# Optimization experiments

Hardware: AMD Instinct MI355X
Metric: run time of the kernel (lower is better)

The kernel has to match this reference:

```python
import jax, jax.numpy as jnp
import numpy as np
import math

B, N, C, S, H, E = 2, 20000, 512, 128, 8, 320000
D = C // H
EPS = 1e-6


def setup_inputs() -> dict:
    key = jax.random.key(0)
    ks = jax.random.split(key, 14)
    x = jax.random.normal(ks[0], (B, N, C), jnp.float32)
    adj_indices = jax.random.randint(ks[1], (2, E), 0, N)
    adj_values = jax.random.uniform(ks[2], (E,), jnp.float32)

    def lin(k, fi, fo):
        # stored as (in, out) so y = x @ W + b (equivalent to torch Linear)
        return jax.random.normal(k, (fi, fo), jnp.float32) / np.sqrt(fi).astype(np.float32)

    Ws = lin(ks[3], C, S); bs = jnp.zeros((S,), jnp.float32)
    Wq = lin(ks[4], C, C); bq = jnp.zeros((C,), jnp.float32)
    Wk = lin(ks[5], C, C); bk = jnp.zeros((C,), jnp.float32)
    Wv = lin(ks[6], C, C); bv = jnp.zeros((C,), jnp.float32)
    Wo = lin(ks[7], C, C); bo = jnp.zeros((C,), jnp.float32)
    beta_raw = jnp.float32(math.log(math.expm1(0.13)))
    return {"x": x, "adj_indices": adj_indices, "adj_values": adj_values,
            "Ws": Ws, "bs": bs, "Wq": Wq, "bq": bq, "Wk": Wk, "bk": bk,
            "Wv": Wv, "bv": bv, "Wo": Wo, "bo": bo, "beta_raw": beta_raw}


def reference(x, adj_indices, adj_values, Ws, bs, Wq, bq, Wk, bk, Wv, bv, Wo, bo, beta_raw):
    # slice assignment weights: (B, N, S)
    weights = jax.nn.softmax(x @ Ws + bs, axis=-1)
    # weight_sum -> (B, S, 1), clamped
    wsum = jnp.maximum(weights.sum(axis=1), EPS)[:, :, None]
    slices = jnp.einsum('bns,bnc->bsc', weights, x) / wsum  # (B, S, C)

    # sparse adjacency aggregation: y[b, r] = sum_e v_e * weights[b, col_e]
    rows, cols = adj_indices[0], adj_indices[1]
    msg = jnp.take(weights, cols, axis=1) * adj_values[None, :, None]  # (B, E, S)
    graph_weights = jax.vmap(lambda m: jax.ops.segment_sum(m, rows, num_segments=N))(msg)  # (B, N, S)

    gb = jnp.einsum('bns,bnt->bst', weights, graph_weights)  # (B, S, S)
    gb = 0.5 * (gb + jnp.swapaxes(gb, 1, 2))
    gb = gb / jnp.maximum(gb.sum(axis=-1, keepdims=True), EPS)
    gb = jnp.log(jnp.maximum(gb, EPS))

    def heads(t, W, b):
        return (t @ W + b).reshape(B, S, H, D).transpose(0, 2, 1, 3)  # (B, H, S, D)

    q = heads(slices, Wq, bq)
    k = heads(slices, Wk, bk)
    v = heads(slices, Wv, bv)
    logits = jnp.einsum('bhqd,bhkd->bhqk', q, k) / math.sqrt(D)
    logits = logits + jax.nn.softplus(beta_raw) * gb[:, None]
    attn = jax.nn.softmax(logits, axis=-1)
    slices_out = jnp.einsum('bhqk,bhkd->bhqd', attn, v).transpose(0, 2, 1, 3).reshape(B, S, C)
    slices_out = slices_out @ Wo + bo
    return jnp.einsum('bns,bsc->bnc', weights, slices_out)  # (B, N, C)
```

## Files before the change

kernel.cpp:

```cpp
#include <hip/hip_runtime.h>
#include <math.h>

#define Bn 2
#define Nn 20000
#define Cn 512
#define Sn 128
#define Hn 8
#define Dn 64
#define En 320000
#define EPSf 1e-6f
#define NB128 157

#define S_CHUNK 640
#define S_KB 32
#define G_CHUNK 256
#define G_KB 79

typedef __attribute__((ext_vector_type(4))) float f32x4;
typedef __attribute__((ext_vector_type(8))) short s16x8;

__device__ __forceinline__ unsigned short f2bf(float f) {
    unsigned u = __float_as_uint(f);
    return (unsigned short)((u + 0x7fffu + ((u >> 16) & 1u)) >> 16);
}
__device__ __forceinline__ float bf2f(unsigned short h) {
    return __uint_as_float(((unsigned)h) << 16);
}

__device__ __forceinline__ unsigned lds_off(int row, int n) {
    unsigned ch = ((((unsigned)n >> 3) ^ ((unsigned)row & 7u) ^ (((unsigned)row >> 3) & 7u)) & 7u);
    return (unsigned)row * 128u + ch * 16u + ((unsigned)n & 7u) * 2u;
}

__device__ __forceinline__ void stage_bf16tile(
    const unsigned short* __restrict__ src, int stride, int nvalid, unsigned* dst, int t)
{
    #pragma unroll
    for (int l = 0; l < 2; l++) {
        int task = t + l * 256;
        int row = task >> 2, seg = task & 3;
        s16x8 a = {0,0,0,0,0,0,0,0}, b = {0,0,0,0,0,0,0,0};
        if (row < nvalid) {
            a = *(const s16x8*)(src + (size_t)row * stride + seg * 16);
            b = *(const s16x8*)(src + (size_t)row * stride + seg * 16 + 8);
        }
        *(s16x8*)((char*)dst + lds_off(row, seg * 16)) = a;
        *(s16x8*)((char*)dst + lds_off(row, seg * 16 + 8)) = b;
    }
}

__device__ __forceinline__ void stage_pairtile(
    const unsigned short* __restrict__ src, int stride, int c0,
    int nbase, int nlimit, unsigned* dst, int t)
{
    int c = t & 15;
    int p0 = t >> 4;
    #pragma unroll
    for (int half = 0; half < 2; half++) {
        int pp = p0 + half * 16;
        int nl = 2 * pp;
        int ng = nbase + nl;
        s16x8 a0 = {0,0,0,0,0,0,0,0}, a1 = {0,0,0,0,0,0,0,0};
        if (ng < nlimit)     a0 = *(const s16x8*)(src + (size_t)ng * stride + c0 + 8 * c);
        if (ng + 1 < nlimit) a1 = *(const s16x8*)(src + (size_t)(ng + 1) * stride + c0 + 8 * c);
        #pragma unroll
        for (int i = 0; i < 8; i++) {
            unsigned val = ((unsigned)(unsigned short)a0[i]) |
                           (((unsigned)(unsigned short)a1[i]) << 16);
            dst[lds_off(8 * c + i, nl) >> 2] = val;
        }
    }
}

__global__ __launch_bounds__(256) void k_prepWsT(
    const float* __restrict__ Ws, unsigned short* __restrict__ WsT)
{
    __shared__ float tile[32][33];
    int t = threadIdx.x;
    int k0 = blockIdx.x * 32;
    int s0 = blockIdx.y * 32;
    #pragma unroll
    for (int l = 0; l < 4; l++) {
        int idx = t + l * 256;
        int r = idx >> 5, c = idx & 31;
        tile[r][c] = Ws[(size_t)(k0 + r) * Sn + s0 + c];
    }
    __syncthreads();
    #pragma unroll
    for (int l = 0; l < 4; l++) {
        int idx = t + l * 256;
        int r = idx >> 5, c = idx & 31;
        WsT[(size_t)(s0 + r) * Cn + k0 + c] = f2bf(tile[c][r]);
    }
}

__global__ __launch_bounds__(256) void k_prepWT(
    const float* __restrict__ Wq, const float* __restrict__ Wk,
    const float* __restrict__ Wv, const float* __restrict__ Wo,
    unsigned short* __restrict__ WT)
{
    __shared__ float tile[32][33];
    int t = threadIdx.x;
    int z = blockIdx.z;
    const float* W = (z == 0) ? Wq : (z == 1) ? Wk : (z == 2) ? Wv : Wo;
    unsigned short* dst = WT + (size_t)z * Cn * Cn;
    int k0 = blockIdx.x * 32;
    int c0 = blockIdx.y * 32;
    #pragma unroll
    for (int l = 0; l < 4; l++) {
        int idx = t + l * 256;
        int r = idx >> 5, c = idx & 31;
        tile[r][c] = W[(size_t)(k0 + r) * Cn + c0 + c];
    }
    __syncthreads();
    #pragma unroll
    for (int l = 0; l < 4; l++) {
        int idx = t + l * 256;
        int r = idx >> 5, c = idx & 31;
        dst[(size_t)(c0 + r) * Cn + k0 + c] = f2bf(tile[c][r]);
    }
}

__global__ __launch_bounds__(256) void k_assign2(
    const float* __restrict__ x, const unsigned short* __restrict__ WsT,
    const float* __restrict__ bs, unsigned short* __restrict__ weights,
    unsigned short* __restrict__ xb16, float* __restrict__ wsum)
{
    __shared__ __align__(16) unsigned At32[4096];
    __shared__ __align__(16) unsigned Bt32[4096];
    __shared__ float wsum_loc[128];

    int t = threadIdx.x;
    int lane = t & 63;
    int wid = t >> 6;
    int l15 = lane & 15, lg = lane >> 4;
    int blk = blockIdx.x;
    int b = blk / NB128;
    int rb = blk % NB128;
    int n0 = rb * 128;
    int nvalid = Nn - n0; if (nvalid > 128) nvalid = 128;
    const float* xb = x + (size_t)b * Nn * Cn;
    unsigned short* xb16g = xb16 + (size_t)b * Nn * Cn;

    if (t < 128) wsum_loc[t] = 0.f;

    f32x4 acc[2][8];
    const f32x4 fz = {0.f, 0.f, 0.f, 0.f};
    #pragma unroll
    for (int i = 0; i < 2; i++) {
        #pragma unroll
        for (int j = 0; j < 8; j++) acc[i][j] = fz;
    }

    for (int ks = 0; ks < 8; ks++) {
        #pragma unroll
        for (int l = 0; l < 2; l++) {
            int task = t + l * 256;
            int row = task >> 2, seg = task & 3;
            bool ok = (row < nvalid);
            float v[16];
            if (ok) {
                const float4* p = (const float4*)(xb + (size_t)(n0 + row) * Cn + ks * 64 + seg * 16);
                float4 a = p[0], bq = p[1], c = p[2], d = p[3];
                v[0]=a.x; v[1]=a.y; v[2]=a.z; v[3]=a.w;
                v[4]=bq.x; v[5]=bq.y; v[6]=bq.z; v[7]=bq.w;
                v[8]=c.x; v[9]=c.y; v[10]=c.z; v[11]=c.w;
                v[12]=d.x; v[13]=d.y; v[14]=d.z; v[15]=d.w;
            } else {
                #pragma unroll
                for (int i = 0; i < 16; i++) v[i] = 0.f;
            }
            uint4 u[2];
            #pragma unroll
            for (int h = 0; h < 2; h++) {
                u[h].x = (unsigned)f2bf(v[h*8+0]) | (((unsigned)f2bf(v[h*8+1])) << 16);
                u[h].y = (unsigned)f2bf(v[h*8+2]) | (((unsigned)f2bf(v[h*8+3])) << 16);
                u[h].z = (unsigned)f2bf(v[h*8+4]) | (((unsigned)f2bf(v[h*8+5])) << 16);
                u[h].w = (unsigned)f2bf(v[h*8+6]) | (((unsigned)f2bf(v[h*8+7])) << 16);
                *(uint4*)((char*)At32 + lds_off(row, seg * 16 + h * 8)) = u[h];
            }
            if (ok) {
                uint4* dst = (uint4*)(xb16g + (size_t)(n0 + row) * Cn + ks * 64 + seg * 16);
                dst[0] = u[0]; dst[1] = u[1];
            }
        }
        stage_bf16tile(WsT + ks * 64, Cn, 128, Bt32, t);
        __syncthreads();
        #pragma unroll
        for (int m = 0; m < 2; m++) {
            s16x8 af[2];
            #pragma unroll
            for (int i = 0; i < 2; i++)
                af[i] = *(const s16x8*)((const char*)At32 +
                        lds_off(wid * 32 + i * 16 + l15, m * 32 + lg * 8));
            #pragma unroll
            for (int j = 0; j < 8; j++) {
                s16x8 bf = *(const s16x8*)((const char*)Bt32 +
                        lds_off(j * 16 + l15, m * 32 + lg * 8));
                #pragma unroll
                for (int i = 0; i < 2; i++)
                    acc[i][j] = __builtin_amdgcn_mfma_f32_16x16x32_bf16(
                        af[i], bf, acc[i][j], 0, 0, 0);
            }
        }
        __syncthreads();
    }

    float bsv[8];
    #pragma unroll
    for (int j = 0; j < 8; j++) bsv[j] = bs[j * 16 + l15];

    unsigned short* wb = weights + (size_t)b * Nn * Sn;
    float wacc[8] = {0.f,0.f,0.f,0.f,0.f,0.f,0.f,0.f};
    #pragma unroll
    for (int i = 0; i < 2; i++) {
        #pragma unroll
        for (int r = 0; r < 4; r++) {
            float lv[8];
            #pragma unroll
            for (int j = 0; j < 8; j++) lv[j] = acc[i][j][r] + bsv[j];
            float m = lv[0];
            #pragma unroll
            for (int j = 1; j < 8; j++) m = fmaxf(m, lv[j]);
            m = fmaxf(m, __shfl_xor(m, 1));
            m = fmaxf(m, __shfl_xor(m, 2));
            m = fmaxf(m, __shfl_xor(m, 4));
            m = fmaxf(m, __shfl_xor(m, 8));
            float e[8], sm = 0.f;
            #pragma unroll
            for (int j = 0; j < 8; j++) { e[j] = __expf(lv[j] - m); sm += e[j]; }
            sm += __shfl_xor(sm, 1);
            sm += __shfl_xor(sm, 2);
            sm += __shfl_xor(sm, 4);
            sm += __shfl_xor(sm, 8);
            float inv = 1.f / sm;
            int n = n0 + wid * 32 + i * 16 + lg * 4 + r;
            bool valid = (n < Nn);
            #pragma unroll
            for (int j = 0; j < 8; j++) {
                float w = e[j] * inv;
                if (valid) {
                    wb[(size_t)n * Sn + j * 16 + l15] = f2bf(w);
                    wacc[j] += w;
                }
            }
        }
    }
    #pragma unroll
    for (int j = 0; j < 8; j++) {
        wacc[j] += __shfl_xor(wacc[j], 16);
        wacc[j] += __shfl_xor(wacc[j], 32);
    }
    if (lg == 0) {
        #pragma unroll
        for (int j = 0; j < 8; j++) atomicAdd(&wsum_loc[j * 16 + l15], wacc[j]);
    }
    __syncthreads();
    if (t < 128) atomicAdd(&wsum[b * Sn + t], wsum_loc[t]);
}

__global__ __launch_bounds__(256) void k_deg(
    const int* __restrict__ adj, int* __restrict__ deg)
{
    int e = blockIdx.x * 256 + threadIdx.x;
    if (e < En) atomicAdd(&deg[adj[e]], 1);
}

__global__ __launch_bounds__(1024) void k_scan(
    const int* __restrict__ deg, int* __restrict__ offs)
{
    __shared__ int wsums[16];
    __shared__ int excl[16];
    __shared__ int runsS;
    __shared__ int totS;
    int t = threadIdx.x;
    int lane = t & 63;
    int w = t >> 6;
    if (t == 0) { offs[0] = 0; runsS = 0; }
    __syncthreads();
    for (int base = 0; base < Nn; base += 1024) {
        int v = (base + t < Nn) ? deg[base + t] : 0;
        int sv = v;
        #pragma unroll
        for (int d = 1; d < 64; d <<= 1) {
            int u = __shfl_up(sv, d);
            if (lane >= d) sv += u;
        }
        if (lane == 63) wsums[w] = sv;
        __syncthreads();
        if (t < 16) {
            int xv = wsums[t];
            int sw = xv;
            #pragma unroll
            for (int d = 1; d < 16; d <<= 1) {
                int u = __shfl_up(sw, d);
                if (t >= d) sw += u;
            }
            excl[t] = sw - xv;
            if (t == 15) totS = sw;
        }
        __syncthreads();
        if (base + t < Nn) offs[base + t + 1] = runsS + excl[w] + sv;
        __syncthreads();
        if (t == 0) runsS += totS;
        __syncthreads();
    }
}

__global__ __launch_bounds__(256) void k_fill(
    const int* __restrict__ adj, const float* __restrict__ vals,
    const int* __restrict__ offs, int* __restrict__ cursor,
    int2* __restrict__ epack)
{
    int e = blockIdx.x * 256 + threadIdx.x;
    if (e < En) {
        int r = adj[e];
        int p = atomicAdd(&cursor[r], 1);
        epack[offs[r] + p] = make_int2(adj[En + e], __float_as_int(vals[e]));
    }
}

__global__ __launch_bounds__(128) void k_gather(
    const unsigned short* __restrict__ weights, const int2* __restrict__ epack,
    const int* __restrict__ offs, unsigned short* __restrict__ gwb)
{
    int r = blockIdx.x;
    int s = threadIdx.x;
    int o0 = offs[r], o1 = offs[r + 1];
    const unsigned short* w0 = weights;
    const unsigned short* w1 = weights + (size_t)Nn * Sn;
    float a0 = 0.f, a1 = 0.f;
    int j = o0;
    for (; j + 4 <= o1; j += 4) {
        int2 e0 = epack[j], e1 = epack[j + 1], e2 = epack[j + 2], e3 = epack[j + 3];
        float v0 = __int_as_float(e0.y), v1 = __int_as_float(e1.y);
        float v2 = __int_as_float(e2.y), v3 = __int_as_float(e3.y);
        float p00 = bf2f(w0[(size_t)e0.x * Sn + s]);
        float p01 = bf2f(w1[(size_t)e0.x * Sn + s]);
        float p10 = bf2f(w0[(size_t)e1.x * Sn + s]);
        float p11 = bf2f(w1[(size_t)e1.x * Sn + s]);
        float p20 = bf2f(w0[(size_t)e2.x * Sn + s]);
        float p21 = bf2f(w1[(size_t)e2.x * Sn + s]);
        float p30 = bf2f(w0[(size_t)e3.x * Sn + s]);
        float p31 = bf2f(w1[(size_t)e3.x * Sn + s]);
        a0 += v0 * p00 + v1 * p10 + v2 * p20 + v3 * p30;
        a1 += v0 * p01 + v1 * p11 + v2 * p21 + v3 * p31;
    }
    for (; j < o1; j++) {
        int2 e = epack[j];
        float v = __int_as_float(e.y);
        a0 += v * bf2f(w0[(size_t)e.x * Sn + s]);
        a1 += v * bf2f(w1[(size_t)e.x * Sn + s]);
    }
    gwb[(size_t)r * Sn + s] = f2bf(a0);
    gwb[(size_t)Nn * Sn + (size_t)r * Sn + s] = f2bf(a1);
}

__global__ __launch_bounds__(256) void k_mm(
    const unsigned short* __restrict__ wAall, const unsigned short* __restrict__ Ball,
    int Bstride, int nCb, int kbCount, int chunk,
    float* __restrict__ partial)
{
    __shared__ __align__(16) unsigned At32[4096];
    __shared__ __align__(16) unsigned Bt32[4096];
    int t = threadIdx.x;
    int lane = t & 63;
    int wid = t >> 6;
    int ws = wid & 1, wc = wid >> 1;
    int blk = blockIdx.x;
    int b = blk / (nCb * kbCount);
    int rem = blk % (nCb * kbCount);
    int cb = rem / kbCount;
    int kb = rem % kbCount;
    int n0 = kb * chunk;
    int c0 = cb * 128;
    const unsigned short* wA = wAall + (size_t)b * Nn * Sn;
    const unsigned short* Bsrc = Ball + (size_t)b * Nn * Bstride;

    f32x4 acc[4][4];
    const f32x4 fz = {0.f, 0.f, 0.f, 0.f};
    #pragma unroll
    for (int i = 0; i < 4; i++) {
        #pragma unroll
        for (int j = 0; j < 4; j++) acc[i][j] = fz;
    }

    int l15 = lane & 15, lg = lane >> 4;

    for (int kt = 0; kt < chunk; kt += 64) {
        stage_pairtile(wA, Sn, 0, n0 + kt, Nn, At32, t);
        stage_pairtile(Bsrc, Bstride, c0, n0 + kt, Nn, Bt32, t);
        __syncthreads();
        #pragma unroll
        for (int m = 0; m < 2; m++) {
            s16x8 af[4], bfr[4];
            #pragma unroll
            for (int i = 0; i < 4; i++) {
                int row = ws * 64 + i * 16 + l15;
                af[i] = *(const s16x8*)((const char*)At32 + lds_off(row, m * 32 + lg * 8));
            }
            #pragma unroll
            for (int j = 0; j < 4; j++) {
                int row = wc * 64 + j * 16 + l15;
                bfr[j] = *(const s16x8*)((const char*)Bt32 + lds_off(row, m * 32 + lg * 8));
            }
            #pragma unroll
            for (int i = 0; i < 4; i++) {
                #pragma unroll
                for (int j = 0; j < 4; j++)
                    acc[i][j] = __builtin_amdgcn_mfma_f32_16x16x32_bf16(
                        af[i], bfr[j], acc[i][j], 0, 0, 0);
            }
        }
        __syncthreads();
    }

    float* pp = partial + (size_t)blk * 16384;
    #pragma unroll
    for (int i = 0; i < 4; i++) {
        int srow = ws * 64 + i * 16 + lg * 4;
        #pragma unroll
        for (int j = 0; j < 4; j++) {
            int ccol = wc * 64 + j * 16 + l15;
            #pragma unroll
            for (int r = 0; r < 4; r++)
                pp[(size_t)(srow + r) * 128 + ccol] = acc[i][j][r];
        }
    }
}

__global__ __launch_bounds__(256) void k_reduceS(
    const float* __restrict__ partial, const float* __restrict__ wsum,
    unsigned short* __restrict__ sl16)
{
    int g = blockIdx.x * 256 + threadIdx.x;
    int c = g & 127;
    int s = (g >> 7) & 127;
    int cb = (g >> 14) & 3;
    int b = g >> 16;
    const float* pp = partial + (size_t)(b * 4 + cb) * S_KB * 16384 + (size_t)s * 128 + c;
    float sum = 0.f;
    #pragma unroll 8
    for (int kb = 0; kb < S_KB; kb++) sum += pp[(size_t)kb * 16384];
    sl16[((size_t)b * Sn + s) * Cn + cb * 128 + c] =
        f2bf(sum / fmaxf(wsum[b * Sn + s], EPSf));
}

__global__ __launch_bounds__(256) void k_reduceG(
    const float* __restrict__ partial, float* __restrict__ gb_raw)
{
    int g = blockIdx.x * 256 + threadIdx.x;
    int t2 = g & 127;
    int s = (g >> 7) & 127;
    int b = g >> 14;
    const float* pp = partial + (size_t)b * G_KB * 16384 + (size_t)s * 128 + t2;
    float sum = 0.f;
    #pragma unroll 8
    for (int kb = 0; kb < G_KB; kb++) sum += pp[(size_t)kb * 16384];
    gb_raw[(size_t)b * 16384 + (size_t)s * 128 + t2] = sum;
}

__global__ __launch_bounds__(128) void k_gb_fin(
    const float* __restrict__ gb_raw, float* __restrict__ gb)
{
    int bid = blockIdx.x;
    int b = bid >> 7, i = bid & 127;
    int j = threadIdx.x;
    const float* gr = gb_raw + (size_t)b * Sn * Sn;
    float sym = 0.5f * (gr[i * Sn + j] + gr[j * Sn + i]);
    float sum = sym;
    #pragma unroll
    for (int d = 1; d < 64; d <<= 1) sum += __shfl_xor(sum, d);
    __shared__ float wred[2];
    if ((j & 63) == 0) wred[j >> 6] = sum;
    __syncthreads();
    sum = wred[0] + wred[1];
    float r = fmaxf(sum, EPSf);
    gb[(size_t)b * Sn * Sn + (size_t)i * Sn + j] = logf(fmaxf(sym / r, EPSf));
}

__global__ __launch_bounds__(256) void k_qkv(
    const unsigned short* __restrict__ sl16, const unsigned short* __restrict__ WT,
    const float* __restrict__ bq, const float* __restrict__ bk,
    const float* __restrict__ bv,
    float* __restrict__ q, float* __restrict__ kb, float* __restrict__ vb)
{
    __shared__ __align__(16) unsigned At32[4096];
    __shared__ __align__(16) unsigned Bt32[4096];
    int t = threadIdx.x;
    int lane = t & 63;
    int wid = t >> 6;
    int ws = wid & 1, wc = wid >> 1;
    int l15 = lane & 15, lg = lane >> 4;
    int rb = blockIdx.x, cb = blockIdx.y, sel = blockIdx.z;
    const unsigned short* Bmat = WT + (size_t)sel * Cn * Cn;
    const float* bias = (sel == 0) ? bq : (sel == 1) ? bk : bv;
    float* outp = (sel == 0) ? q : (sel == 1) ? kb : vb;

    f32x4 acc[4][4];
    const f32x4 fz = {0.f, 0.f, 0.f, 0.f};
    #pragma unroll
    for (int i = 0; i < 4; i++) {
        #pragma unroll
        for (int j = 0; j < 4; j++) acc[i][j] = fz;
    }

    for (int ks = 0; ks < 8; ks++) {
        stage_bf16tile(sl16 + (size_t)rb * 128 * Cn + ks * 64, Cn, 128, At32, t);
        stage_bf16tile(Bmat + (size_t)cb * 128 * Cn + ks * 64, Cn, 128, Bt32, t);
        __syncthreads();
        #pragma unroll
        for (int m = 0; m < 2; m++) {
            s16x8 af[4], bfr[4];
            #pragma unroll
            for (int i = 0; i < 4; i++)
                af[i] = *(const s16x8*)((const char*)At32 +
                        lds_off(ws * 64 + i * 16 + l15, m * 32 + lg * 8));
            #pragma unroll
            for (int j = 0; j < 4; j++)
                bfr[j] = *(const s16x8*)((const char*)Bt32 +
                        lds_off(wc * 64 + j * 16 + l15, m * 32 + lg * 8));
            #pragma unroll
            for (int i = 0; i < 4; i++) {
                #pragma unroll
                for (int j = 0; j < 4; j++)
                    acc[i][j] = __builtin_amdgcn_mfma_f32_16x16x32_bf16(
                        af[i], bfr[j], acc[i][j], 0, 0, 0);
            }
        }
        __syncthreads();
    }

    float bvv[4];
    #pragma unroll
    for (int j = 0; j < 4; j++) bvv[j] = bias[cb * 128 + wc * 64 + j * 16 + l15];
    #pragma unroll
    for (int i = 0; i < 4; i++) {
        #pragma unroll
        for (int r = 0; r < 4; r++) {
            int m = rb * 128 + ws * 64 + i * 16 + lg * 4 + r;
            #pragma unroll
            for (int j = 0; j < 4; j++)
                outp[(size_t)m * Cn + cb * 128 + wc * 64 + j * 16 + l15] =
                    acc[i][j][r] + bvv[j];
        }
    }
}

__global__ __launch_bounds__(128) void k_attn(
    const float* __restrict__ q, const float* __restrict__ k,
    const float* __restrict__ v, const float* __restrict__ gb,
    const float* __restrict__ beta_raw, unsigned short* __restrict__ attn16)
{
    __shared__ float kv[128][65];
    __shared__ float qv[64];
    __shared__ float p[128];
    __shared__ float wred[2][2];

    int t = threadIdx.x;
    int bid = blockIdx.x;
    int b = bid / (Hn * Sn);
    int h = (bid / Sn) % Hn;
    int i = bid % Sn;
    size_t base = (size_t)b * Sn * Cn + (size_t)h * Dn;

    if (t < 64) qv[t] = q[base + (size_t)i * Cn + t];
    for (int l = 0; l < 64; l++) {
        int idx = t + l * 128;
        int j = idx >> 6, d = idx & 63;
        kv[j][d] = k[base + (size_t)j * Cn + d];
    }
    __syncthreads();

    float dot = 0.f;
    #pragma unroll
    for (int d = 0; d < 64; d++) dot += qv[d] * kv[t][d];

    float beta = log1pf(__expf(beta_raw[0]));
    float logit = dot * 0.125f + beta * gb[(size_t)b * Sn * Sn + (size_t)i * Sn + t];

    float m = logit;
    #pragma unroll
    for (int d = 1; d < 64; d <<= 1) m = fmaxf(m, __shfl_xor(m, d));
    if ((t & 63) == 0) wred[0][t >> 6] = m;
    __syncthreads();
    m = fmaxf(wred[0][0], wred[0][1]);
    float e = __expf(logit - m);
    float sm = e;
    #pragma unroll
    for (int d = 1; d < 64; d <<= 1) sm += __shfl_xor(sm, d);
    if ((t & 63) == 0) wred[1][t >> 6] = sm;
    __syncthreads();
    sm = wred[1][0] + wred[1][1];
    p[t] = e / sm;
    __syncthreads();

    for (int l = 0; l < 64; l++) {
        int idx = t + l * 128;
        int j = idx >> 6, d = idx & 63;
        kv[j][d] = v[base + (size_t)j * Cn + d];
    }
    __syncthreads();

    if (t < 64) {
        float o = 0.f;
        #pragma unroll 8
        for (int j = 0; j < 128; j++) o += p[j] * kv[j][t];
        attn16[base + (size_t)i * Cn + t] = f2bf(o);
    }
}

__global__ __launch_bounds__(256) void k_wo(
    const unsigned short* __restrict__ attn16, const unsigned short* __restrict__ WoT,
    const float* __restrict__ bo, unsigned short* __restrict__ SoT)
{
    __shared__ __align__(16) unsigned At32[4096];
    __shared__ __align__(16) unsigned Bt32[4096];
    int t = threadIdx.x;
    int lane = t & 63;
    int wid = t >> 6;
    int ws = wid & 1, wc = wid >> 1;
    int l15 = lane & 15, lg = lane >> 4;
    int b = blockIdx.x, cb = blockIdx.y;

    f32x4 acc[4][4];
    const f32x4 fz = {0.f, 0.f, 0.f, 0.f};
    #pragma unroll
    for (int i = 0; i < 4; i++) {
        #pragma unroll
        for (int j = 0; j < 4; j++) acc[i][j] = fz;
    }

    for (int ks = 0; ks < 8; ks++) {
        stage_bf16tile(attn16 + (size_t)b * 128 * Cn + ks * 64, Cn, 128, At32, t);
        stage_bf16tile(WoT + (size_t)cb * 128 * Cn + ks * 64, Cn, 128, Bt32, t);
        __syncthreads();
        #pragma unroll
        for (int m = 0; m < 2; m++) {
            s16x8 af[4], bfr[4];
            #pragma unroll
            for (int i = 0; i < 4; i++)
                af[i] = *(const s16x8*)((const char*)At32 +
                        lds_off(ws * 64 + i * 16 + l15, m * 32 + lg * 8));
            #pragma unroll
            for (int j = 0; j < 4; j++)
                bfr[j] = *(const s16x8*)((const char*)Bt32 +
                        lds_off(wc * 64 + j * 16 + l15, m * 32 + lg * 8));
            #pragma unroll
            for (int i = 0; i < 4; i++) {
                #pragma unroll
                for (int j = 0; j < 4; j++)
                    acc[i][j] = __builtin_amdgcn_mfma_f32_16x16x32_bf16(
                        af[i], bfr[j], acc[i][j], 0, 0, 0);
            }
        }
        __syncthreads();
    }

    float bvv[4];
    #pragma unroll
    for (int j = 0; j < 4; j++) bvv[j] = bo[cb * 128 + wc * 64 + j * 16 + l15];
    unsigned short* sb = SoT + (size_t)b * Cn * Sn;
    #pragma unroll
    for (int i = 0; i < 4; i++) {
        #pragma unroll
        for (int j = 0; j < 4; j++) {
            int c = cb * 128 + wc * 64 + j * 16 + l15;
            #pragma unroll
            for (int r = 0; r < 4; r++) {
                int s = ws * 64 + i * 16 + lg * 4 + r;
                sb[(size_t)c * Sn + s] = f2bf(acc[i][j][r] + bvv[j]);
            }
        }
    }
}

__global__ __launch_bounds__(256) void k_out2(
    const unsigned short* __restrict__ wAll, const unsigned short* __restrict__ SoT,
    float* __restrict__ out)
{
    __shared__ __align__(16) unsigned At32[4096];
    __shared__ __align__(16) unsigned Bt32[4096];
    int t = threadIdx.x;
    int lane = t & 63;
    int wid = t >> 6;
    int ws = wid & 1, wc = wid >> 1;
    int l15 = lane & 15, lg = lane >> 4;
    int blk = blockIdx.x;
    int b = blk / (NB128 * 4);
    int rem = blk % (NB128 * 4);
    int rb = rem >> 2;
    int cb = rem & 3;
    int n0 = rb * 128, c0 = cb * 128;
    int nvalid = Nn - n0; if (nvalid > 128) nvalid = 128;
    const unsigned short* wb = wAll + (size_t)b * Nn * Sn;
    const unsigned short* sb = SoT + (size_t)b * Cn * Sn;

    f32x4 acc[4][4];
    const f32x4 fz = {0.f, 0.f, 0.f, 0.f};
    #pragma unroll
    for (int i = 0; i < 4; i++) {
        #pragma unroll
        for (int j = 0; j < 4; j++) acc[i][j] = fz;
    }

    #pragma unroll
    for (int ksi = 0; ksi < 2; ksi++) {
        stage_bf16tile(wb + (size_t)n0 * Sn + ksi * 64, Sn, nvalid, At32, t);
        stage_bf16tile(sb + (size_t)c0 * Sn + ksi * 64, Sn, 128, Bt32, t);
        __syncthreads();
        #pragma unroll
        for (int m = 0; m < 2; m++) {
            s16x8 af[4], bfr[4];
            #pragma unroll
            for (int i = 0; i < 4; i++)
                af[i] = *(const s16x8*)((const char*)At32 +
                        lds_off(ws * 64 + i * 16 + l15, m * 32 + lg * 8));
            #pragma unroll
            for (int j = 0; j < 4; j++)
                bfr[j] = *(const s16x8*)((const char*)Bt32 +
                        lds_off(wc * 64 + j * 16 + l15, m * 32 + lg * 8));
            #pragma unroll
            for (int i = 0; i < 4; i++) {
                #pragma unroll
                for (int j = 0; j < 4; j++)
                    acc[i][j] = __builtin_amdgcn_mfma_f32_16x16x32_bf16(
                        af[i], bfr[j], acc[i][j], 0, 0, 0);
            }
        }
        __syncthreads();
    }

    #pragma unroll
    for (int i = 0; i < 4; i++) {
        #pragma unroll
        for (int r = 0; r < 4; r++) {
            int n = n0 + ws * 64 + i * 16 + lg * 4 + r;
            if (n < Nn) {
                #pragma unroll
                for (int j = 0; j < 4; j++)
                    out[((size_t)b * Nn + n) * Cn + c0 + wc * 64 + j * 16 + l15] =
                        acc[i][j][r];
            }
        }
    }
}

extern "C" void kernel_launch(void* const* d_in, const int* in_sizes, int n_in,
                              void* d_out, int out_size, void* d_ws, size_t ws_size,
                              hipStream_t stream)
{
    const float* x  = (const float*)d_in[0];
    const int* adj  = (const int*)d_in[1];
    const float* av = (const float*)d_in[2];
    const float* Ws = (const float*)d_in[3];
    const float* bs = (const float*)d_in[4];
    const float* Wq = (const float*)d_in[5];
    const float* bq = (const float*)d_in[6];
    const float* Wk = (const float*)d_in[7];
    const float* bk = (const float*)d_in[8];
    const float* Wv = (const float*)d_in[9];
    const float* bv = (const float*)d_in[10];
    const float* Wo = (const float*)d_in[11];
    const float* bo = (const float*)d_in[12];
    const float* br = (const float*)d_in[13];
    float* out = (float*)d_out;
    (void)in_sizes; (void)n_in; (void)out_size; (void)ws_size;

    char* ws = (char*)d_ws;
    size_t off = 0;
    unsigned short* wb16  = (unsigned short*)(ws + off); off += (size_t)Bn * Nn * Sn * 2;
    unsigned short* xb16  = (unsigned short*)(ws + off); off += (size_t)Bn * Nn * Cn * 2;
    unsigned short* gwb16 = (unsigned short*)(ws + off); off += (size_t)Bn * Nn * Sn * 2;
    unsigned short* sl16  = (unsigned short*)(ws + off); off += (size_t)Bn * Sn * Cn * 2;
    float* wsum       = (float*)(ws + off); off += 1024;
    float* gb_raw     = (float*)(ws + off); off += (size_t)Bn * Sn * Sn * 4;
    float* gb         = (float*)(ws + off); off += (size_t)Bn * Sn * Sn * 4;
    float* q          = (float*)(ws + off); off += (size_t)Bn * Sn * Cn * 4;
    float* kbuf       = (float*)(ws + off); off += (size_t)Bn * Sn * Cn * 4;
    float* vbuf       = (float*)(ws + off); off += (size_t)Bn * Sn * Cn * 4;
    unsigned short* attn16 = (unsigned short*)(ws + off); off += (size_t)Bn * Sn * Cn * 2;
    unsigned short* WsT = (unsigned short*)(ws + off); off += (size_t)Sn * Cn * 2;
    unsigned short* WT  = (unsigned short*)(ws + off); off += (size_t)4 * Cn * Cn * 2;
    unsigned short* SoT = (unsigned short*)(ws + off); off += (size_t)Bn * Cn * Sn * 2;
    char* U = ws + off;
    int*  deg    = (int*)(U);
    int*  cursor = (int*)(U + 80128);
    int*  offs   = (int*)(U + 160256);
    int2* epack  = (int2*)(U + 240640);
    float* partialS = (float*)U;
    float* partialG = (float*)U;

    hipMemsetAsync(wsum, 0, 1024, stream);
    hipMemsetAsync(U, 0, 160256, stream);

    k_prepWsT<<<dim3(16, 4), 256, 0, stream>>>(Ws, WsT);
    k_prepWT<<<dim3(16, 16, 4), 256, 0, stream>>>(Wq, Wk, Wv, Wo, WT);
    k_assign2<<<Bn * NB128, 256, 0, stream>>>(x, WsT, bs, wb16, xb16, wsum);

    k_deg<<<(En + 255) / 256, 256, 0, stream>>>(adj, deg);
    k_scan<<<1, 1024, 0, stream>>>(deg, offs);
    k_fill<<<(En + 255) / 256, 256, 0, stream>>>(adj, av, offs, cursor, epack);
    k_gather<<<Nn, 128, 0, stream>>>(wb16, epack, offs, gwb16);

    k_mm<<<Bn * 4 * S_KB, 256, 0, stream>>>(wb16, xb16, Cn, 4, S_KB, S_CHUNK, partialS);
    k_reduceS<<<(Bn * Sn * Cn) / 256, 256, 0, stream>>>(partialS, wsum, sl16);

    k_mm<<<Bn * G_KB, 256, 0, stream>>>(wb16, gwb16, Sn, 1, G_KB, G_CHUNK, partialG);
    k_reduceG<<<(Bn * Sn * Sn) / 256, 256, 0, stream>>>(partialG, gb_raw);
    k_gb_fin<<<Bn * Sn, 128, 0, stream>>>(gb_raw, gb);

    k_qkv<<<dim3(2, 4, 3), 256, 0, stream>>>(sl16, WT, bq, bk, bv, q, kbuf, vbuf);
    k_attn<<<Bn * Hn * Sn, 128, 0, stream>>>(q, kbuf, vbuf, gb, br, attn16);
    k_wo<<<dim3(2, 4), 256, 0, stream>>>(attn16, WT + (size_t)3 * Cn * Cn, bo, SoT);

    k_out2<<<Bn * NB128 * 4, 256, 0, stream>>>(wb16, SoT, out);
}
```

Baseline: 263.9 us.

## Drop bf16 copy of x; convert fp32 x on the fly in slice GEMM

Removes the bf16 copy of x that the assignment kernel used to write to global memory. The slice aggregation GEMM now reads fp32 x directly and converts it to bf16 while staging into LDS. The assignment kernel is shrunk to 64-row blocks for more blocks, and the split-K chunk sizes for both reduction GEMMs are halved to raise parallelism, which doubles the number of partials to reduce. The trade is one fewer 20 MB write plus its reread, against a doubled fp32 read of x in the GEMM and more partial-sum traffic.

```diff
diff --git a/kernel.cpp b/kernel.cpp
--- a/kernel.cpp
+++ b/kernel.cpp
@@ -9,12 +9,13 @@
 #define Dn 64
 #define En 320000
 #define EPSf 1e-6f
+#define NB64 313
 #define NB128 157
 
-#define S_CHUNK 640
-#define S_KB 32
-#define G_CHUNK 256
-#define G_KB 79
+#define S_CHUNK 320
+#define S_KB 63
+#define G_CHUNK 128
+#define G_KB 157
 
 typedef __attribute__((ext_vector_type(4))) float f32x4;
 typedef __attribute__((ext_vector_type(8))) short s16x8;
@@ -72,6 +73,53 @@
     }
 }
 
+__device__ __forceinline__ void stage_tilesF(
+    const unsigned short* __restrict__ wA, const float* __restrict__ Bsrc,
+    int Bstride, int c0, int nbase, unsigned* At32, unsigned* Bt32, int t)
+{
+    int c = t & 15;
+    int p0 = t >> 4;
+    #pragma unroll
+    for (int half = 0; half < 2; half++) {
+        int pp = p0 + half * 16;
+        int nl = 2 * pp;
+        int ng = nbase + nl;
+        s16x8 a0 = {0,0,0,0,0,0,0,0}, a1 = {0,0,0,0,0,0,0,0};
+        if (ng < Nn)     a0 = *(const s16x8*)(wA + (size_t)ng * Sn + 8 * c);
+        if (ng + 1 < Nn) a1 = *(const s16x8*)(wA + (size_t)(ng + 1) * Sn + 8 * c);
+        #pragma unroll
+        for (int i = 0; i < 8; i++) {
+            unsigned val = ((unsigned)(unsigned short)a0[i]) |
+                           (((unsigned)(unsigned short)a1[i]) << 16);
+            At32[lds_off(8 * c + i, nl) >> 2] = val;
+        }
+        float b0[8], b1[8];
+        if (ng < Nn) {
+            float4 v0 = *(const float4*)(Bsrc + (size_t)ng * Bstride + c0 + 8 * c);
+            float4 v1 = *(const float4*)(Bsrc + (size_t)ng * Bstride + c0 + 8 * c + 4);
+            b0[0]=v0.x; b0[1]=v0.y; b0[2]=v0.z; b0[3]=v0.w;
+            b0[4]=v1.x; b0[5]=v1.y; b0[6]=v1.z; b0[7]=v1.w;
+        } else {
+            #pragma unroll
+            for (int i = 0; i < 8; i++) b0[i] = 0.f;
+        }
+        if (ng + 1 < Nn) {
+            float4 v0 = *(const float4*)(Bsrc + (size_t)(ng + 1) * Bstride + c0 + 8 * c);
+            float4 v1 = *(const float4*)(Bsrc + (size_t)(ng + 1) * Bstride + c0 + 8 * c + 4);
+            b1[0]=v0.x; b1[1]=v0.y; b1[2]=v0.z; b1[3]=v0.w;
+            b1[4]=v1.x; b1[5]=v1.y; b1[6]=v1.z; b1[7]=v1.w;
+        } else {
+            #pragma unroll
+            for (int i = 0; i < 8; i++) b1[i] = 0.f;
+        }
+        #pragma unroll
+        for (int i = 0; i < 8; i++) {
+            unsigned val = (unsigned)f2bf(b0[i]) | (((unsigned)f2bf(b1[i])) << 16);
+            Bt32[lds_off(8 * c + i, nl) >> 2] = val;
+        }
+    }
+}
+
 __global__ __launch_bounds__(256) void k_prepWsT(
     const float* __restrict__ Ws, unsigned short* __restrict__ WsT)
 {
@@ -124,9 +172,9 @@
 __global__ __launch_bounds__(256) void k_assign2(
     const float* __restrict__ x, const unsigned short* __restrict__ WsT,
     const float* __restrict__ bs, unsigned short* __restrict__ weights,
-    unsigned short* __restrict__ xb16, float* __restrict__ wsum)
-{
-    __shared__ __align__(16) unsigned At32[4096];
+    float* __restrict__ wsum)
+{
+    __shared__ __align__(16) unsigned At32[2048];
     __shared__ __align__(16) unsigned Bt32[4096];
     __shared__ float wsum_loc[128];
 
@@ -135,31 +183,24 @@
     int wid = t >> 6;
     int l15 = lane & 15, lg = lane >> 4;
     int blk = blockIdx.x;
-    int b = blk / NB128;
-    int rb = blk % NB128;
-    int n0 = rb * 128;
-    int nvalid = Nn - n0; if (nvalid > 128) nvalid = 128;
+    int b = blk / NB64;
+    int rb = blk % NB64;
+    int n0 = rb * 64;
+    int nvalid = Nn - n0; if (nvalid > 64) nvalid = 64;
     const float* xb = x + (size_t)b * Nn * Cn;
-    unsigned short* xb16g = xb16 + (size_t)b * Nn * Cn;
 
     if (t < 128) wsum_loc[t] = 0.f;
 
-    f32x4 acc[2][8];
+    f32x4 acc[8];
     const f32x4 fz = {0.f, 0.f, 0.f, 0.f};
     #pragma unroll
-    for (int i = 0; i < 2; i++) {
-        #pragma unroll
-        for (int j = 0; j < 8; j++) acc[i][j] = fz;
-    }
+    for (int j = 0; j < 8; j++) acc[j] = fz;
 
     for (int ks = 0; ks < 8; ks++) {
-        #pragma unroll
-        for (int l = 0; l < 2; l++) {
-            int task = t + l * 256;
-            int row = task >> 2, seg = task & 3;
-            bool ok = (row < nvalid);
+        {
+            int row = t >> 2, seg = t & 3;
             float v[16];
-            if (ok) {
+            if (row < nvalid) {
                 const float4* p = (const float4*)(xb + (size_t)(n0 + row) * Cn + ks * 64 + seg * 16);
                 float4 a = p[0], bq = p[1], c = p[2], d = p[3];
                 v[0]=a.x; v[1]=a.y; v[2]=a.z; v[3]=a.w;
@@ -170,37 +211,27 @@
                 #pragma unroll
                 for (int i = 0; i < 16; i++) v[i] = 0.f;
             }
-            uint4 u[2];
             #pragma unroll
             for (int h = 0; h < 2; h++) {
-                u[h].x = (unsigned)f2bf(v[h*8+0]) | (((unsigned)f2bf(v[h*8+1])) << 16);
-                u[h].y = (unsigned)f2bf(v[h*8+2]) | (((unsigned)f2bf(v[h*8+3])) << 16);
-                u[h].z = (unsigned)f2bf(v[h*8+4]) | (((unsigned)f2bf(v[h*8+5])) << 16);
-                u[h].w = (unsigned)f2bf(v[h*8+6]) | (((unsigned)f2bf(v[h*8+7])) << 16);
-                *(uint4*)((char*)At32 + lds_off(row, seg * 16 + h * 8)) = u[h];
-            }
-            if (ok) {
-                uint4* dst = (uint4*)(xb16g + (size_t)(n0 + row) * Cn + ks * 64 + seg * 16);
-                dst[0] = u[0]; dst[1] = u[1];
+                uint4 u;
+                u.x = (unsigned)f2bf(v[h*8+0]) | (((unsigned)f2bf(v[h*8+1])) << 16);
+                u.y = (unsigned)f2bf(v[h*8+2]) | (((unsigned)f2bf(v[h*8+3])) << 16);
+                u.z = (unsigned)f2bf(v[h*8+4]) | (((unsigned)f2bf(v[h*8+5])) << 16);
+                u.w = (unsigned)f2bf(v[h*8+6]) | (((unsigned)f2bf(v[h*8+7])) << 16);
+                *(uint4*)((char*)At32 + lds_off(row, seg * 16 + h * 8)) = u;
             }
         }
         stage_bf16tile(WsT + ks * 64, Cn, 128, Bt32, t);
         __syncthreads();
         #pragma unroll
         for (int m = 0; m < 2; m++) {
-            s16x8 af[2];
-            #pragma unroll
-            for (int i = 0; i < 2; i++)
-                af[i] = *(const s16x8*)((const char*)At32 +
-                        lds_off(wid * 32 + i * 16 + l15, m * 32 + lg * 8));
+            s16x8 af = *(const s16x8*)((const char*)At32 +
+                       lds_off(wid * 16 + l15, m * 32 + lg * 8));
             #pragma unroll
             for (int j = 0; j < 8; j++) {
                 s16x8 bf = *(const s16x8*)((const char*)Bt32 +
-                        lds_off(j * 16 + l15, m * 32 + lg * 8));
-                #pragma unroll
-                for (int i = 0; i < 2; i++)
-                    acc[i][j] = __builtin_amdgcn_mfma_f32_16x16x32_bf16(
-                        af[i], bf, acc[i][j], 0, 0, 0);
+                           lds_off(j * 16 + l15, m * 32 + lg * 8));
+                acc[j] = __builtin_amdgcn_mfma_f32_16x16x32_bf16(af, bf, acc[j], 0, 0, 0);
             }
         }
         __syncthreads();
@@ -213,36 +244,33 @@
     unsigned short* wb = weights + (size_t)b * Nn * Sn;
     float wacc[8] = {0.f,0.f,0.f,0.f,0.f,0.f,0.f,0.f};
     #pragma unroll
-    for (int i = 0; i < 2; i++) {
-        #pragma unroll
-        for (int r = 0; r < 4; r++) {
-            float lv[8];
-            #pragma unroll
-            for (int j = 0; j < 8; j++) lv[j] = acc[i][j][r] + bsv[j];
-            float m = lv[0];
-            #pragma unroll
-            for (int j = 1; j < 8; j++) m = fmaxf(m, lv[j]);
-            m = fmaxf(m, __shfl_xor(m, 1));
-            m = fmaxf(m, __shfl_xor(m, 2));
-            m = fmaxf(m, __shfl_xor(m, 4));
-            m = fmaxf(m, __shfl_xor(m, 8));
-            float e[8], sm = 0.f;
-            #pragma unroll
-            for (int j = 0; j < 8; j++) { e[j] = __expf(lv[j] - m); sm += e[j]; }
-            sm += __shfl_xor(sm, 1);
-            sm += __shfl_xor(sm, 2);
-            sm += __shfl_xor(sm, 4);
-            sm += __shfl_xor(sm, 8);
-            float inv = 1.f / sm;
-            int n = n0 + wid * 32 + i * 16 + lg * 4 + r;
-            bool valid = (n < Nn);
-            #pragma unroll
-            for (int j = 0; j < 8; j++) {
-                float w = e[j] * inv;
-                if (valid) {
-                    wb[(size_t)n * Sn + j * 16 + l15] = f2bf(w);
-                    wacc[j] += w;
-                }
+    for (int r = 0; r < 4; r++) {
+        float lv[8];
+        #pragma unroll
+        for (int j = 0; j < 8; j++) lv[j] = acc[j][r] + bsv[j];
+        float m = lv[0];
+        #pragma unroll
+        for (int j = 1; j < 8; j++) m = fmaxf(m, lv[j]);
+        m = fmaxf(m, __shfl_xor(m, 1));
+        m = fmaxf(m, __shfl_xor(m, 2));
+        m = fmaxf(m, __shfl_xor(m, 4));
+        m = fmaxf(m, __shfl_xor(m, 8));
+        float e[8], sm = 0.f;
+        #pragma unroll
+        for (int j = 0; j < 8; j++) { e[j] = __expf(lv[j] - m); sm += e[j]; }
+        sm += __shfl_xor(sm, 1);
+        sm += __shfl_xor(sm, 2);
+        sm += __shfl_xor(sm, 4);
+        sm += __shfl_xor(sm, 8);
+        float inv = 1.f / sm;
+        int n = n0 + wid * 16 + lg * 4 + r;
+        bool valid = (n < Nn);
+        #pragma unroll
+        for (int j = 0; j < 8; j++) {
+            float w = e[j] * inv;
+            if (valid) {
+                wb[(size_t)n * Sn + j * 16 + l15] = f2bf(w);
+                wacc[j] += w;
             }
         }
     }
@@ -356,9 +384,8 @@
     gwb[(size_t)Nn * Sn + (size_t)r * Sn + s] = f2bf(a1);
 }
 
-__global__ __launch_bounds__(256) void k_mm(
-    const unsigned short* __restrict__ wAall, const unsigned short* __restrict__ Ball,
-    int Bstride, int nCb, int kbCount, int chunk,
+__global__ __launch_bounds__(256) void k_mmS(
+    const unsigned short* __restrict__ wAall, const float* __restrict__ xall,
     float* __restrict__ partial)
 {
     __shared__ __align__(16) unsigned At32[4096];
@@ -368,14 +395,14 @@
     int wid = t >> 6;
     int ws = wid & 1, wc = wid >> 1;
     int blk = blockIdx.x;
-    int b = blk / (nCb * kbCount);
-    int rem = blk % (nCb * kbCount);
-    int cb = rem / kbCount;
-    int kb = rem % kbCount;
-    int n0 = kb * chunk;
+    int b = blk / (4 * S_KB);
+    int rem = blk % (4 * S_KB);
+    int cb = rem / S_KB;
+    int kb = rem % S_KB;
+    int n0 = kb * S_CHUNK;
     int c0 = cb * 128;
     const unsigned short* wA = wAall + (size_t)b * Nn * Sn;
-    const unsigned short* Bsrc = Ball + (size_t)b * Nn * Bstride;
+    const float* Bsrc = xall + (size_t)b * Nn * Cn;
 
     f32x4 acc[4][4];
     const f32x4 fz = {0.f, 0.f, 0.f, 0.f};
@@ -387,9 +414,77 @@
 
     int l15 = lane & 15, lg = lane >> 4;
 
-    for (int kt = 0; kt < chunk; kt += 64) {
+    for (int kt = 0; kt < S_CHUNK; kt += 64) {
+        stage_tilesF(wA, Bsrc, Cn, c0, n0 + kt, At32, Bt32, t);
+        __syncthreads();
+        #pragma unroll
+        for (int m = 0; m < 2; m++) {
+            s16x8 af[4], bfr[4];
+            #pragma unroll
+            for (int i = 0; i < 4; i++) {
+                int row = ws * 64 + i * 16 + l15;
+                af[i] = *(const s16x8*)((const char*)At32 + lds_off(row, m * 32 + lg * 8));
+            }
+            #pragma unroll
+            for (int j = 0; j < 4; j++) {
+                int row = wc * 64 + j * 16 + l15;
+                bfr[j] = *(const s16x8*)((const char*)Bt32 + lds_off(row, m * 32 + lg * 8));
+            }
+            #pragma unroll
+            for (int i = 0; i < 4; i++) {
+                #pragma unroll
+                for (int j = 0; j < 4; j++)
+                    acc[i][j] = __builtin_amdgcn_mfma_f32_16x16x32_bf16(
+                        af[i], bfr[j], acc[i][j], 0, 0, 0);
+            }
+        }
+        __syncthreads();
+    }
+
+    float* pp = partial + (size_t)blk * 16384;
+    #pragma unroll
+    for (int i = 0; i < 4; i++) {
+        int srow = ws * 64 + i * 16 + lg * 4;
+        #pragma unroll
+        for (int j = 0; j < 4; j++) {
+            int ccol = wc * 64 + j * 16 + l15;
+            #pragma unroll
+            for (int r = 0; r < 4; r++)
+                pp[(size_t)(srow + r) * 128 + ccol] = acc[i][j][r];
+        }
+    }
+}
+
+__global__ __launch_bounds__(256) void k_mmG(
+    const unsigned short* __restrict__ wAall, const unsigned short* __restrict__ gwall,
+    float* __restrict__ partial)
+{
+    __shared__ __align__(16) unsigned At32[4096];
+    __shared__ __align__(16) unsigned Bt32[4096];
+    int t = threadIdx.x;
+    int lane = t & 63;
+    int wid = t >> 6;
+    int ws = wid & 1, wc = wid >> 1;
+    int blk = blockIdx.x;
+    int b = blk / G_KB;
+    int kb = blk % G_KB;
+    int n0 = kb * G_CHUNK;
+    const unsigned short* wA = wAall + (size_t)b * Nn * Sn;
+    const unsigned short* Bsrc = gwall + (size_t)b * Nn * Sn;
+
+    f32x4 acc[4][4];
+    const f32x4 fz = {0.f, 0.f, 0.f, 0.f};
+    #pragma unroll
+    for (int i = 0; i < 4; i++) {
+        #pragma unroll
+        for (int j = 0; j < 4; j++) acc[i][j] = fz;
+    }
+
+    int l15 = lane & 15, lg = lane >> 4;
+
+    for (int kt = 0; kt < G_CHUNK; kt += 64) {
         stage_pairtile(wA, Sn, 0, n0 + kt, Nn, At32, t);
-        stage_pairtile(Bsrc, Bstride, c0, n0 + kt, Nn, Bt32, t);
+        stage_pairtile(Bsrc, Sn, 0, n0 + kt, Nn, Bt32, t);
         __syncthreads();
         #pragma unroll
         for (int m = 0; m < 2; m++) {
@@ -440,7 +535,7 @@
     int b = g >> 16;
     const float* pp = partial + (size_t)(b * 4 + cb) * S_KB * 16384 + (size_t)s * 128 + c;
     float sum = 0.f;
-    #pragma unroll 8
+    #pragma unroll 7
     for (int kb = 0; kb < S_KB; kb++) sum += pp[(size_t)kb * 16384];
     sl16[((size_t)b * Sn + s) * Cn + cb * 128 + c] =
         f2bf(sum / fmaxf(wsum[b * Sn + s], EPSf));
@@ -770,7 +865,6 @@
     char* ws = (char*)d_ws;
     size_t off = 0;
     unsigned short* wb16  = (unsigned short*)(ws + off); off += (size_t)Bn * Nn * Sn * 2;
-    unsigned short* xb16  = (unsigned short*)(ws + off); off += (size_t)Bn * Nn * Cn * 2;
     unsigned short* gwb16 = (unsigned short*)(ws + off); off += (size_t)Bn * Nn * Sn * 2;
     unsigned short* sl16  = (unsigned short*)(ws + off); off += (size_t)Bn * Sn * Cn * 2;
     float* wsum       = (float*)(ws + off); off += 1024;
@@ -796,17 +890,17 @@
 
     k_prepWsT<<<dim3(16, 4), 256, 0, stream>>>(Ws, WsT);
     k_prepWT<<<dim3(16, 16, 4), 256, 0, stream>>>(Wq, Wk, Wv, Wo, WT);
-    k_assign2<<<Bn * NB128, 256, 0, stream>>>(x, WsT, bs, wb16, xb16, wsum);
+    k_assign2<<<Bn * NB64, 256, 0, stream>>>(x, WsT, bs, wb16, wsum);
 
     k_deg<<<(En + 255) / 256, 256, 0, stream>>>(adj, deg);
     k_scan<<<1, 1024, 0, stream>>>(deg, offs);
     k_fill<<<(En + 255) / 256, 256, 0, stream>>>(adj, av, offs, cursor, epack);
     k_gather<<<Nn, 128, 0, stream>>>(wb16, epack, offs, gwb16);
 
-    k_mm<<<Bn * 4 * S_KB, 256, 0, stream>>>(wb16, xb16, Cn, 4, S_KB, S_CHUNK, partialS);
+    k_mmS<<<Bn * 4 * S_KB, 256, 0, stream>>>(wb16, x, partialS);
     k_reduceS<<<(Bn * Sn * Cn) / 256, 256, 0, stream>>>(partialS, wsum, sl16);
 
-    k_mm<<<Bn * G_KB, 256, 0, stream>>>(wb16, gwb16, Sn, 1, G_KB, G_CHUNK, partialG);
+    k_mmG<<<Bn * G_KB, 256, 0, stream>>>(wb16, gwb16, partialG);
     k_reduceG<<<(Bn * Sn * Sn) / 256, 256, 0, stream>>>(partialG, gb_raw);
     k_gb_fin<<<Bn * Sn, 128, 0, stream>>>(gb_raw, gb);
 
```

Measured after the change: 256.2 us. 2.9% less time.
